# Optimization experiments

Measured on AMD Instinct MI355X. Metric: run time of the kernel, lower is better.

The kernel has to match this reference:

```python
import jax, jax.numpy as jnp
import numpy as np

B, T, I, H = 4096, 512, 4, 64  # batch, seq_len, input_size, hidden_size


def setup_inputs() -> dict:
    key = jax.random.key(0)
    ks = jax.random.split(key, 13)
    sc = 1.0 / np.sqrt(H)
    sc2 = 1.0 / np.sqrt(32)
    n = lambda k, shape, s: (jax.random.normal(k, shape, jnp.float32) * s)
    return {
        "x": jax.random.normal(ks[0], (B, T, I), jnp.float32),
        # PyTorch LSTM layout: gates stacked as [i, f, g, o] along first dim
        "w_ih0": n(ks[1], (4 * H, I), sc),
        "w_hh0": n(ks[2], (4 * H, H), sc),
        "b_ih0": n(ks[3], (4 * H,), sc),
        "b_hh0": n(ks[4], (4 * H,), sc),
        "w_ih1": n(ks[5], (4 * H, H), sc),
        "w_hh1": n(ks[6], (4 * H, H), sc),
        "b_ih1": n(ks[7], (4 * H,), sc),
        "b_hh1": n(ks[8], (4 * H,), sc),
        "fc1_w": n(ks[9], (32, H), sc),
        "fc1_b": n(ks[10], (32,), sc),
        "fc2_w": n(ks[11], (2, 32), sc2),
        "fc2_b": n(ks[12], (2,), sc2),
    }


def _lstm_layer(x, w_ih, w_hh, b_ih, b_hh):
    # x: [B, T, D_in] -> hidden sequence [B, T, H]
    Bq = x.shape[0]
    Hq = w_hh.shape[1]
    # Precompute input contribution for all timesteps in one GEMM
    pre = jnp.einsum('bti,gi->btg', x, w_ih) + b_ih + b_hh  # [B, T, 4H]
    pre = jnp.swapaxes(pre, 0, 1)  # [T, B, 4H] for scan

    def step(carry, xt):
        h, c = carry
        gates = xt + h @ w_hh.T  # [B, 4H]
        i, f, g, o = jnp.split(gates, 4, axis=-1)
        c_new = jax.nn.sigmoid(f) * c + jax.nn.sigmoid(i) * jnp.tanh(g)
        h_new = jax.nn.sigmoid(o) * jnp.tanh(c_new)
        return (h_new, c_new), h_new

    h0 = jnp.zeros((Bq, Hq), x.dtype)
    _, hs = jax.lax.scan(step, (h0, h0), pre)
    return jnp.swapaxes(hs, 0, 1)  # [B, T, H]


def reference(x, w_ih0, w_hh0, b_ih0, b_hh0, w_ih1, w_hh1, b_ih1, b_hh1,
              fc1_w, fc1_b, fc2_w, fc2_b):
    h1 = _lstm_layer(x, w_ih0, w_hh0, b_ih0, b_hh0)
    # dropout(p=0.2) between LSTM layers is inactive in eval mode
    h2 = _lstm_layer(h1, w_ih1, w_hh1, b_ih1, b_hh1)
    last = h2[:, -1, :]  # [B, H]
    y = jax.nn.relu(last @ fc1_w.T + fc1_b)
    return jax.nn.relu(y @ fc2_w.T + fc2_b)  # [B, 2]
```

## Files before the change

### kernel.cpp

```cpp
#include <hip/hip_runtime.h>

#define TT 512
#define MM 16

typedef _Float16 f16_t;
typedef f16_t f16x8 __attribute__((ext_vector_type(8)));
typedef float  f32x4 __attribute__((ext_vector_type(4)));

#define MFMA16(A, B, C) __builtin_amdgcn_mfma_f32_16x16x32_f16((A), (B), (C), 0, 0, 0)

__device__ __forceinline__ float fr(float x) { return __builtin_amdgcn_rcpf(x); }

#if __has_builtin(__builtin_amdgcn_exp2f)
__device__ __forceinline__ float ex2(float x) { return __builtin_amdgcn_exp2f(x); }
#define EXS 1.44269504f
#else
__device__ __forceinline__ float ex2(float x) { return __expf(x); }
#define EXS 1.0f
#endif

__device__ __forceinline__ float cellEW(float pi, float pf, float pg, float po,
                                        float4 bsc, float& c) {
    float A = ex2(fmaf(pf, -EXS, bsc.y));
    float B = ex2(fmaf(pi, -EXS, bsc.x));
    float C = ex2(fmaf(pg, 2.f * EXS, bsc.z));
    float u   = (1.f + B) * (C + 1.f);
    float oa  = 1.f + A;
    float num = fmaf(c * oa, u * fr(oa), oa * (C - 1.f));
    float cn;
    {
        float nm = fmaf(c, u, oa * (C - 1.f));
        float den = oa * u;
        cn = nm * fr(den);
    }
    (void)num;
    c = cn;
    float D = ex2(fmaf(po, -EXS, bsc.w));
    float E = ex2(2.f * EXS * cn);
    float rd = fr(1.f + D);
    float re = fr(E + 1.f);
    return rd * fmaf(-2.f, re, 1.f);
}

__device__ __forceinline__ f16x8 cvt8(const float* p) {
    f16x8 r;
#pragma unroll
    for (int e = 0; e < 8; ++e) r[e] = (f16_t)p[e];
    return r;
}

__device__ __forceinline__ f16x8 buildxf(float4 xq, int lq) {
    float v[4] = {xq.x, xq.y, xq.z, xq.w};
    f16x8 r;
#pragma unroll
    for (int e = 0; e < 8; ++e) r[e] = (e < 4 && lq == 0) ? (f16_t)v[e] : (f16_t)0.f;
    return r;
}


__global__ __launch_bounds__(512, 2) void lstm_hs(
    const float* __restrict__ x,
    const float* __restrict__ w_ih0, const float* __restrict__ w_hh0,
    const float* __restrict__ b_ih0, const float* __restrict__ b_hh0,
    const float* __restrict__ w_ih1, const float* __restrict__ w_hh1,
    const float* __restrict__ b_ih1, const float* __restrict__ b_hh1,
    const float* __restrict__ fc1_w, const float* __restrict__ fc1_b,
    const float* __restrict__ fc2_w, const float* __restrict__ fc2_b,
    float* __restrict__ out)
{
    __shared__ __align__(16) unsigned hp1[2][512];
    __shared__ __align__(16) unsigned hp2[512];
    __shared__ __align__(16) float sH[MM * 68];
    __shared__ float sY[MM * 34];

    const int tid = threadIdx.x;
    const int l   = tid & 63;
    const int wv  = tid >> 6;
    const int rbase = blockIdx.x * MM;

    const int lc = l & 15;
    const int lq = l >> 4;
    const int chunk = l ^ lq;

    const bool isL1 = (wv >= 4);
    const int  ht   = wv & 3;
    const int  hidx = ht * 16 + lc;

    const int ktw = hidx >> 5;
    const int kk  = hidx & 31;
    const int ew  = kk & 7;
    const int kb  = kk >> 3;

    f16x8 wA[4][2], wB[4][2], wx[4];
    float bb[4];
#pragma unroll
    for (int g = 0; g < 4; ++g) {
        const int ga = g * 64 + hidx;
        if (isL1) {
#pragma unroll
            for (int kt = 0; kt < 2; ++kt)
                wA[g][kt] = cvt8(w_hh0 + ga * 64 + kt * 32 + lq * 8);
            float4 w4 = *(const float4*)(w_ih0 + ga * 4);
            wx[g] = buildxf(w4, lq);
            bb[g] = b_ih0[ga] + b_hh0[ga];
        } else {
#pragma unroll
            for (int kt = 0; kt < 2; ++kt) {
                wA[g][kt] = cvt8(w_ih1 + ga * 64 + kt * 32 + lq * 8);
                wB[g][kt] = cvt8(w_hh1 + ga * 64 + kt * 32 + lq * 8);
            }
            bb[g] = b_ih1[ga] + b_hh1[ga];
        }
    }
    const float4 bsc = make_float4(-EXS * bb[0], -EXS * bb[1],
                                   2.f * EXS * bb[2], -EXS * bb[3]);

    hp2[tid] = 0;

    float c_st[4] = {0.f, 0.f, 0.f, 0.f};

    const float4* xg = (const float4*)x;
    const size_t xrow = (size_t)(rbase + lc) * TT;
    float4 xq = make_float4(0, 0, 0, 0), xq0 = make_float4(0, 0, 0, 0);
    if (isL1) { xq0 = xg[xrow + 0]; xq = xg[xrow + 1]; }

    __syncthreads();

    if (isL1) {
        f16x8 xf = buildxf(xq0, lq);
        f32x4 a[4];
#pragma unroll
        for (int g = 0; g < 4; ++g) {
#pragma unroll
            for (int q = 0; q < 4; ++q) a[g][q] = 0.f;
            a[g] = MFMA16(xf, wx[g], a[g]);
        }
        f16_t* dst = (f16_t*)hp1[0];
#pragma unroll
        for (int q = 0; q < 4; ++q) {
            float hv = cellEW(a[0][q], a[1][q], a[2][q], a[3][q], bsc, c_st[q]);
            const int lp = (lq * 4 + q) + 16 * kb;
            dst[ktw * 512 + (lp ^ kb) * 8 + ew] = (f16_t)hv;
        }
    }
    __syncthreads();

    int p = 0;
    f32x4 a2[4];
    for (int t = 0; t < TT; ++t) {
        f32x4 a1[4];
        if (isL1) {
            if (t + 1 < TT) {
                const int tn = (t + 2 < TT) ? t + 2 : TT - 1;
                float4 xn = xg[xrow + tn];

                const f16_t* p1 = (const f16_t*)hp1[p];
                f16x8 ah[2];
#pragma unroll
                for (int kt = 0; kt < 2; ++kt)
                    ah[kt] = *(const f16x8*)(p1 + kt * 512 + chunk * 8);
                f16x8 xf = buildxf(xq, lq);

                __builtin_amdgcn_s_setprio(1);
#pragma unroll
                for (int g = 0; g < 4; ++g) {
#pragma unroll
                    for (int q = 0; q < 4; ++q) a1[g][q] = 0.f;
                    a1[g] = MFMA16(xf, wx[g], a1[g]);
                    a1[g] = MFMA16(ah[0], wA[g][0], a1[g]);
                    a1[g] = MFMA16(ah[1], wA[g][1], a1[g]);
                }
                __builtin_amdgcn_s_setprio(0);
                xq = xn;
            }
        } else {
            if (t >= 1) {
                f16_t* dst = (f16_t*)hp2;
#pragma unroll
                for (int q = 0; q < 4; ++q) {
                    float hv = cellEW(a2[0][q], a2[1][q], a2[2][q], a2[3][q], bsc, c_st[q]);
                    const int lp = (lq * 4 + q) + 16 * kb;
                    dst[ktw * 512 + (lp ^ kb) * 8 + ew] = (f16_t)hv;
                }
            }
        }
        __syncthreads();

        if (isL1) {
            if (t + 1 < TT) {
                f16_t* dst = (f16_t*)hp1[p ^ 1];
#pragma unroll
                for (int q = 0; q < 4; ++q) {
                    float hv = cellEW(a1[0][q], a1[1][q], a1[2][q], a1[3][q], bsc, c_st[q]);
                    const int lp = (lq * 4 + q) + 16 * kb;
                    dst[ktw * 512 + (lp ^ kb) * 8 + ew] = (f16_t)hv;
                }
            }
        } else {
            const f16_t* p1 = (const f16_t*)hp1[p];
            const f16_t* p2 = (const f16_t*)hp2;
            f16x8 ah[2], ph[2];
#pragma unroll
            for (int kt = 0; kt < 2; ++kt) {
                ah[kt] = *(const f16x8*)(p1 + kt * 512 + chunk * 8);
                ph[kt] = *(const f16x8*)(p2 + kt * 512 + chunk * 8);
            }
            __builtin_amdgcn_s_setprio(1);
#pragma unroll
            for (int g = 0; g < 4; ++g) {
#pragma unroll
                for (int q = 0; q < 4; ++q) a2[g][q] = 0.f;
                a2[g] = MFMA16(ah[0], wA[g][0], a2[g]);
                a2[g] = MFMA16(ah[1], wA[g][1], a2[g]);
                a2[g] = MFMA16(ph[0], wB[g][0], a2[g]);
                a2[g] = MFMA16(ph[1], wB[g][1], a2[g]);
            }
            __builtin_amdgcn_s_setprio(0);
        }
        p ^= 1;
        __syncthreads();
    }

    if (!isL1) {
#pragma unroll
        for (int q = 0; q < 4; ++q) {
            float hv = cellEW(a2[0][q], a2[1][q], a2[2][q], a2[3][q], bsc, c_st[q]);
            sH[(lq * 4 + q) * 68 + hidx] = hv;
        }
    }
    __syncthreads();

    {
        const int r = tid >> 5, mo = tid & 31;
        float s = fc1_b[mo];
#pragma unroll 8
        for (int k = 0; k < 64; ++k) s = fmaf(sH[r * 68 + k], fc1_w[mo * 64 + k], s);
        sY[r * 34 + mo] = fmaxf(s, 0.f);
    }
    __syncthreads();
    if (tid < 32) {
        const int r = tid >> 1, o = tid & 1;
        float s = fc2_b[o];
#pragma unroll 8
        for (int mo = 0; mo < 32; ++mo) s = fmaf(sY[r * 34 + mo], fc2_w[o * 32 + mo], s);
        out[(size_t)(rbase + r) * 2 + o] = fmaxf(s, 0.f);
    }
}

extern "C" void kernel_launch(void* const* d_in, const int* in_sizes, int n_in,
                              void* d_out, int out_size, void* d_ws, size_t ws_size,
                              hipStream_t stream) {
    const float* x     = (const float*)d_in[0];
    const float* w_ih0 = (const float*)d_in[1];
    const float* w_hh0 = (const float*)d_in[2];
    const float* b_ih0 = (const float*)d_in[3];
    const float* b_hh0 = (const float*)d_in[4];
    const float* w_ih1 = (const float*)d_in[5];
    const float* w_hh1 = (const float*)d_in[6];
    const float* b_ih1 = (const float*)d_in[7];
    const float* b_hh1 = (const float*)d_in[8];
    const float* fc1_w = (const float*)d_in[9];
    const float* fc1_b = (const float*)d_in[10];
    const float* fc2_w = (const float*)d_in[11];
    const float* fc2_b = (const float*)d_in[12];
    float* out = (float*)d_out;

    const int nB   = in_sizes[0] / (TT * 4);
    const int grid = nB / MM;

    lstm_hs<<<grid, 512, 0, stream>>>(x, w_ih0, w_hh0, b_ih0, b_hh0,
                                      w_ih1, w_hh1, b_ih1, b_hh1,
                                      fc1_w, fc1_b, fc2_w, fc2_b, out);
}
```

Baseline: 451.9 us.

## Merge both LSTM layers into each wave using half-filled MFMA rows

Each block now takes 8 batch rows with 256 threads (4 waves), not 16 rows with 8 waves. Every wave holds the weights of both layers and issues both layers' MFMAs each step. The layer-2 preactivations are moved into the upper 32 lanes by a shuffle, so half the lanes run the layer-1 cell update and half run layer 2. This doubles the grid and the block count, and removes the separate producer and consumer waves and one barrier per step. In exchange it wastes half the MFMA M rows (8 of 16 active), raises register pressure from three weight sets per wave, and adds an s_sleep for blocks at index 256 and above.

Result: slower. 598.8 us (+32.5%).

```diff
diff --git a/kernel.cpp b/kernel.cpp
--- a/kernel.cpp
+++ b/kernel.cpp
@@ -1,7 +1,7 @@
 #include <hip/hip_runtime.h>
 
 #define TT 512
-#define MM 16
+#define MM 8
 
 typedef _Float16 f16_t;
 typedef f16_t f16x8 __attribute__((ext_vector_type(8)));
@@ -24,22 +24,13 @@
     float A = ex2(fmaf(pf, -EXS, bsc.y));
     float B = ex2(fmaf(pi, -EXS, bsc.x));
     float C = ex2(fmaf(pg, 2.f * EXS, bsc.z));
-    float u   = (1.f + B) * (C + 1.f);
-    float oa  = 1.f + A;
-    float num = fmaf(c * oa, u * fr(oa), oa * (C - 1.f));
-    float cn;
-    {
-        float nm = fmaf(c, u, oa * (C - 1.f));
-        float den = oa * u;
-        cn = nm * fr(den);
-    }
-    (void)num;
+    float oa = 1.f + A;
+    float u  = (1.f + B) * (C + 1.f);
+    float cn = fmaf(c, u, oa * (C - 1.f)) * fr(oa * u);
     c = cn;
     float D = ex2(fmaf(po, -EXS, bsc.w));
     float E = ex2(2.f * EXS * cn);
-    float rd = fr(1.f + D);
-    float re = fr(E + 1.f);
-    return rd * fmaf(-2.f, re, 1.f);
+    return fr(1.f + D) * fmaf(-2.f, fr(E + 1.f), 1.f);
 }
 
 __device__ __forceinline__ f16x8 cvt8(const float* p) {
@@ -49,16 +40,17 @@
     return r;
 }
 
-__device__ __forceinline__ f16x8 buildxf(float4 xq, int lq) {
+__device__ __forceinline__ f16x8 buildxf(float4 xq, int lq, int lc) {
     float v[4] = {xq.x, xq.y, xq.z, xq.w};
     f16x8 r;
 #pragma unroll
-    for (int e = 0; e < 8; ++e) r[e] = (e < 4 && lq == 0) ? (f16_t)v[e] : (f16_t)0.f;
+    for (int e = 0; e < 8; ++e)
+        r[e] = (e < 4 && lq == 0 && lc < 8) ? (f16_t)v[e] : (f16_t)0.f;
     return r;
 }
 
 
-__global__ __launch_bounds__(512, 2) void lstm_hs(
+__global__ __launch_bounds__(256, 2) void lstm_2b(
     const float* __restrict__ x,
     const float* __restrict__ w_ih0, const float* __restrict__ w_hh0,
     const float* __restrict__ b_ih0, const float* __restrict__ b_hh0,
@@ -68,8 +60,7 @@
     const float* __restrict__ fc2_w, const float* __restrict__ fc2_b,
     float* __restrict__ out)
 {
-    __shared__ __align__(16) unsigned hp1[2][512];
-    __shared__ __align__(16) unsigned hp2[512];
+    __shared__ __align__(16) unsigned hpl[4][512];
     __shared__ __align__(16) float sH[MM * 68];
     __shared__ float sY[MM * 34];
 
@@ -81,154 +72,123 @@
     const int lc = l & 15;
     const int lq = l >> 4;
     const int chunk = l ^ lq;
-
-    const bool isL1 = (wv >= 4);
-    const int  ht   = wv & 3;
-    const int  hidx = ht * 16 + lc;
-
+    const int hidx = wv * 16 + lc;
+
+    const int rgrp = (l >> 4) & 1;
+    const bool isl2 = (l >= 32);
     const int ktw = hidx >> 5;
-    const int kk  = hidx & 31;
-    const int ew  = kk & 7;
-    const int kb  = kk >> 3;
-
-    f16x8 wA[4][2], wB[4][2], wx[4];
-    float bb[4];
-#pragma unroll
-    for (int g = 0; g < 4; ++g) {
-        const int ga = g * 64 + hidx;
-        if (isL1) {
-#pragma unroll
-            for (int kt = 0; kt < 2; ++kt)
-                wA[g][kt] = cvt8(w_hh0 + ga * 64 + kt * 32 + lq * 8);
+    const int kb  = (hidx & 31) >> 3;
+    const int ew  = hidx & 7;
+
+    f16x8 wA0[4][2], wx[4], wA1[4][2], wB1[4][2];
+    float4 bsc_ew;
+    {
+        float b0[4], b1[4];
+#pragma unroll
+        for (int g = 0; g < 4; ++g) {
+            const int ga = g * 64 + hidx;
+#pragma unroll
+            for (int kt = 0; kt < 2; ++kt) {
+                wA0[g][kt] = cvt8(w_hh0 + ga * 64 + kt * 32 + lq * 8);
+                wA1[g][kt] = cvt8(w_ih1 + ga * 64 + kt * 32 + lq * 8);
+                wB1[g][kt] = cvt8(w_hh1 + ga * 64 + kt * 32 + lq * 8);
+            }
             float4 w4 = *(const float4*)(w_ih0 + ga * 4);
-            wx[g] = buildxf(w4, lq);
-            bb[g] = b_ih0[ga] + b_hh0[ga];
-        } else {
-#pragma unroll
-            for (int kt = 0; kt < 2; ++kt) {
-                wA[g][kt] = cvt8(w_ih1 + ga * 64 + kt * 32 + lq * 8);
-                wB[g][kt] = cvt8(w_hh1 + ga * 64 + kt * 32 + lq * 8);
+            float v[4] = {w4.x, w4.y, w4.z, w4.w};
+#pragma unroll
+            for (int e = 0; e < 8; ++e)
+                wx[g][e] = (e < 4 && lq == 0) ? (f16_t)v[e] : (f16_t)0.f;
+            b0[g] = b_ih0[ga] + b_hh0[ga];
+            b1[g] = b_ih1[ga] + b_hh1[ga];
+        }
+        float bi = isl2 ? b1[0] : b0[0];
+        float bf = isl2 ? b1[1] : b0[1];
+        float bg = isl2 ? b1[2] : b0[2];
+        float bo = isl2 ? b1[3] : b0[3];
+        bsc_ew = make_float4(-EXS * bi, -EXS * bf, 2.f * EXS * bg, -EXS * bo);
+    }
+
+    for (int i = tid; i < 4 * 512; i += 256) ((unsigned*)hpl)[i] = 0;
+
+    float c_st[4] = {0.f, 0.f, 0.f, 0.f};
+    const f32x4 z4 = {0.f, 0.f, 0.f, 0.f};
+
+    const float4* xg = (const float4*)x;
+    const size_t xrow = (size_t)(rbase + (lc & 7)) * TT;
+    float4 xq0 = xg[xrow + 0];
+    float4 xq  = xg[xrow + 1];
+
+    if (blockIdx.x >= 256) __builtin_amdgcn_s_sleep(5);
+
+    __syncthreads();
+
+    {
+        f16x8 xf0 = buildxf(xq0, lq, lc);
+        f32x4 ap[4];
+#pragma unroll
+        for (int g = 0; g < 4; ++g) ap[g] = MFMA16(xf0, wx[g], z4);
+        if (l < 32) {
+            f16_t* dst = (f16_t*)hpl[0];
+#pragma unroll
+            for (int c = 0; c < 4; ++c) {
+                float hv = cellEW(ap[0][c], ap[1][c], ap[2][c], ap[3][c], bsc_ew, c_st[c]);
+                const int lp = (rgrp * 4 + c) + 16 * kb;
+                dst[ktw * 512 + (lp ^ kb) * 8 + ew] = (f16_t)hv;
             }
-            bb[g] = b_ih1[ga] + b_hh1[ga];
-        }
-    }
-    const float4 bsc = make_float4(-EXS * bb[0], -EXS * bb[1],
-                                   2.f * EXS * bb[2], -EXS * bb[3]);
-
-    hp2[tid] = 0;
-
-    float c_st[4] = {0.f, 0.f, 0.f, 0.f};
-
-    const float4* xg = (const float4*)x;
-    const size_t xrow = (size_t)(rbase + lc) * TT;
-    float4 xq = make_float4(0, 0, 0, 0), xq0 = make_float4(0, 0, 0, 0);
-    if (isL1) { xq0 = xg[xrow + 0]; xq = xg[xrow + 1]; }
-
+        }
+    }
     __syncthreads();
 
-    if (isL1) {
-        f16x8 xf = buildxf(xq0, lq);
-        f32x4 a[4];
+    int p = 0;
+    for (int t = 0; t < TT; ++t) {
+        const int tn = (t + 2 < TT) ? t + 2 : TT - 1;
+        float4 xn = xg[xrow + tn];
+
+        const f16_t* p1 = (const f16_t*)hpl[p];
+        const f16_t* p2 = (const f16_t*)hpl[2 + p];
+        f16x8 ah0 = *(const f16x8*)(p1 + chunk * 8);
+        f16x8 ah1 = *(const f16x8*)(p1 + 512 + chunk * 8);
+        f16x8 ph0 = *(const f16x8*)(p2 + chunk * 8);
+        f16x8 ph1 = *(const f16x8*)(p2 + 512 + chunk * 8);
+        f16x8 xf  = buildxf(xq, lq, lc);
+
+        f32x4 a1[4], a2[4];
+        __builtin_amdgcn_s_setprio(1);
 #pragma unroll
         for (int g = 0; g < 4; ++g) {
-#pragma unroll
-            for (int q = 0; q < 4; ++q) a[g][q] = 0.f;
-            a[g] = MFMA16(xf, wx[g], a[g]);
-        }
-        f16_t* dst = (f16_t*)hp1[0];
-#pragma unroll
-        for (int q = 0; q < 4; ++q) {
-            float hv = cellEW(a[0][q], a[1][q], a[2][q], a[3][q], bsc, c_st[q]);
-            const int lp = (lq * 4 + q) + 16 * kb;
+            a1[g] = MFMA16(xf, wx[g], z4);
+            a1[g] = MFMA16(ah0, wA0[g][0], a1[g]);
+            a1[g] = MFMA16(ah1, wA0[g][1], a1[g]);
+            a2[g] = MFMA16(ah0, wA1[g][0], z4);
+            a2[g] = MFMA16(ah1, wA1[g][1], a2[g]);
+            a2[g] = MFMA16(ph0, wB1[g][0], a2[g]);
+            a2[g] = MFMA16(ph1, wB1[g][1], a2[g]);
+        }
+        __builtin_amdgcn_s_setprio(0);
+
+        float pre[4][4];
+#pragma unroll
+        for (int g = 0; g < 4; ++g) {
+#pragma unroll
+            for (int c = 0; c < 4; ++c) {
+                float tmp = __shfl(a2[g][c], l & 31);
+                pre[g][c] = isl2 ? tmp : a1[g][c];
+            }
+        }
+
+        f16_t* dst = (f16_t*)hpl[isl2 ? (2 + (p ^ 1)) : (p ^ 1)];
+        const bool last = (t == TT - 1);
+#pragma unroll
+        for (int c = 0; c < 4; ++c) {
+            float hv = cellEW(pre[0][c], pre[1][c], pre[2][c], pre[3][c], bsc_ew, c_st[c]);
+            const int lp = (rgrp * 4 + c) + 16 * kb;
             dst[ktw * 512 + (lp ^ kb) * 8 + ew] = (f16_t)hv;
-        }
-    }
-    __syncthreads();
-
-    int p = 0;
-    f32x4 a2[4];
-    for (int t = 0; t < TT; ++t) {
-        f32x4 a1[4];
-        if (isL1) {
-            if (t + 1 < TT) {
-                const int tn = (t + 2 < TT) ? t + 2 : TT - 1;
-                float4 xn = xg[xrow + tn];
-
-                const f16_t* p1 = (const f16_t*)hp1[p];
-                f16x8 ah[2];
-#pragma unroll
-                for (int kt = 0; kt < 2; ++kt)
-                    ah[kt] = *(const f16x8*)(p1 + kt * 512 + chunk * 8);
-                f16x8 xf = buildxf(xq, lq);
-
-                __builtin_amdgcn_s_setprio(1);
-#pragma unroll
-                for (int g = 0; g < 4; ++g) {
-#pragma unroll
-                    for (int q = 0; q < 4; ++q) a1[g][q] = 0.f;
-                    a1[g] = MFMA16(xf, wx[g], a1[g]);
-                    a1[g] = MFMA16(ah[0], wA[g][0], a1[g]);
-                    a1[g] = MFMA16(ah[1], wA[g][1], a1[g]);
-                }
-                __builtin_amdgcn_s_setprio(0);
-                xq = xn;
-            }
-        } else {
-            if (t >= 1) {
-                f16_t* dst = (f16_t*)hp2;
-#pragma unroll
-                for (int q = 0; q < 4; ++q) {
-                    float hv = cellEW(a2[0][q], a2[1][q], a2[2][q], a2[3][q], bsc, c_st[q]);
-                    const int lp = (lq * 4 + q) + 16 * kb;
-                    dst[ktw * 512 + (lp ^ kb) * 8 + ew] = (f16_t)hv;
-                }
-            }
-        }
-        __syncthreads();
-
-        if (isL1) {
-            if (t + 1 < TT) {
-                f16_t* dst = (f16_t*)hp1[p ^ 1];
-#pragma unroll
-                for (int q = 0; q < 4; ++q) {
-                    float hv = cellEW(a1[0][q], a1[1][q], a1[2][q], a1[3][q], bsc, c_st[q]);
-                    const int lp = (lq * 4 + q) + 16 * kb;
-                    dst[ktw * 512 + (lp ^ kb) * 8 + ew] = (f16_t)hv;
-                }
-            }
-        } else {
-            const f16_t* p1 = (const f16_t*)hp1[p];
-            const f16_t* p2 = (const f16_t*)hp2;
-            f16x8 ah[2], ph[2];
-#pragma unroll
-            for (int kt = 0; kt < 2; ++kt) {
-                ah[kt] = *(const f16x8*)(p1 + kt * 512 + chunk * 8);
-                ph[kt] = *(const f16x8*)(p2 + kt * 512 + chunk * 8);
-            }
-            __builtin_amdgcn_s_setprio(1);
-#pragma unroll
-            for (int g = 0; g < 4; ++g) {
-#pragma unroll
-                for (int q = 0; q < 4; ++q) a2[g][q] = 0.f;
-                a2[g] = MFMA16(ah[0], wA[g][0], a2[g]);
-                a2[g] = MFMA16(ah[1], wA[g][1], a2[g]);
-                a2[g] = MFMA16(ph[0], wB[g][0], a2[g]);
-                a2[g] = MFMA16(ph[1], wB[g][1], a2[g]);
-            }
-            __builtin_amdgcn_s_setprio(0);
-        }
+            if (last && isl2) sH[(rgrp * 4 + c) * 68 + hidx] = hv;
+        }
+        xq = xn;
         p ^= 1;
         __syncthreads();
     }
-
-    if (!isL1) {
-#pragma unroll
-        for (int q = 0; q < 4; ++q) {
-            float hv = cellEW(a2[0][q], a2[1][q], a2[2][q], a2[3][q], bsc, c_st[q]);
-            sH[(lq * 4 + q) * 68 + hidx] = hv;
-        }
-    }
-    __syncthreads();
 
     {
         const int r = tid >> 5, mo = tid & 31;
@@ -238,7 +198,7 @@
         sY[r * 34 + mo] = fmaxf(s, 0.f);
     }
     __syncthreads();
-    if (tid < 32) {
+    if (tid < MM * 2) {
         const int r = tid >> 1, o = tid & 1;
         float s = fc2_b[o];
 #pragma unroll 8
@@ -268,7 +228,7 @@
     const int nB   = in_sizes[0] / (TT * 4);
     const int grid = nB / MM;
 
-    lstm_hs<<<grid, 512, 0, stream>>>(x, w_ih0, w_hh0, b_ih0, b_hh0,
+    lstm_2b<<<grid, 256, 0, stream>>>(x, w_ih0, w_hh0, b_ih0, b_hh0,
                                       w_ih1, w_hh1, b_ih1, b_hh1,
                                       fc1_w, fc1_b, fc2_w, fc2_b, out);
 }
```
